# Performance work log

Measured on AMD Instinct MI355X. Metric: run time of the kernel, lower is better.

## Reference

```python
import jax, jax.numpy as jnp
import numpy as np

EMBED_DIM = 128
B, N = 8, 2048


def entmax15(z):
    """Exact 1.5-entmax along the last axis (Peters & Martins 2019, sort-based)."""
    z = z / 2.0
    z = z - jnp.max(z, axis=-1, keepdims=True)  # shift-invariance -> numerical stability
    zs = -jnp.sort(-z, axis=-1)                 # descending sort
    n = z.shape[-1]
    k = jnp.arange(1, n + 1, dtype=z.dtype)
    mean = jnp.cumsum(zs, axis=-1) / k
    meansq = jnp.cumsum(zs * zs, axis=-1) / k
    ss = k * (meansq - mean * mean)
    delta = (1.0 - ss) / k
    delta_safe = jnp.where(delta > 0, delta, 1.0)
    tau = mean - jnp.where(delta > 0, jnp.sqrt(delta_safe), 0.0)
    support = jnp.sum((tau <= zs).astype(jnp.int32), axis=-1, keepdims=True)
    tau_star = jnp.take_along_axis(tau, support - 1, axis=-1)
    return jnp.square(jnp.maximum(z - tau_star, 0.0))


def setup_inputs() -> dict:
    key = jax.random.key(0)
    ks = jax.random.split(key, 6)
    s = 1.0 / np.sqrt(EMBED_DIM)  # torch nn.Linear default init range
    return {
        "x_c": jax.random.normal(ks[0], (B, N, EMBED_DIM), jnp.float32),
        "x_n": jax.random.normal(ks[1], (B, N, EMBED_DIM), jnp.float32),
        "Wq": jax.random.uniform(ks[2], (EMBED_DIM, EMBED_DIM), jnp.float32, -s, s),
        "bq": jax.random.uniform(ks[3], (EMBED_DIM,), jnp.float32, -s, s),
        "Wk": jax.random.uniform(ks[4], (EMBED_DIM, EMBED_DIM), jnp.float32, -s, s),
        "bk": jax.random.uniform(ks[5], (EMBED_DIM,), jnp.float32, -s, s),
    }


def reference(x_c, x_n, Wq, bq, Wk, bk):
    Q = x_c @ Wq.T + bq                      # [B,N,D]
    K = x_n @ Wk.T + bk                      # [B,N,D]
    A = jnp.einsum("bnd,bmd->bnm", Q, K) / jnp.sqrt(jnp.float32(EMBED_DIM))
    # entmax15 sparse normalization over keys; dropout is identity in eval mode
    return entmax15(A)
```

## Files before the change

kernel.cpp:

```cpp
#include <hip/hip_runtime.h>
#include <hip/hip_bf16.h>

#define BATCH 8
#define SEQ   2048
#define DIM   128
#define NROWS 16384
#define THETA_SPAN 22.62741699796952f

typedef __bf16    bf16x8   __attribute__((ext_vector_type(8)));
typedef float     floatx16 __attribute__((ext_vector_type(16)));
typedef _Float16  half2v   __attribute__((ext_vector_type(2)));

static __device__ __forceinline__ unsigned short f2bf(float v) {
    union { __hip_bfloat16 h; unsigned short u; } c;
    c.h = __float2bfloat16(v);
    return c.u;
}
static __device__ __forceinline__ float bf2f(unsigned short u) {
    union { unsigned int i; float f; } c;
    c.i = (unsigned int)u << 16;
    return c.f;
}
static __device__ __forceinline__ unsigned short f2h(float v) {
    union { _Float16 h; unsigned short u; } c;
    c.h = (_Float16)v;
    return c.u;
}

#if __has_builtin(__builtin_amdgcn_fdot2)
static __device__ __forceinline__ float fdot2acc(half2v a, half2v b, float c) {
    return __builtin_amdgcn_fdot2(a, b, c, false);
}
#else
static __device__ __forceinline__ float fdot2acc(half2v a, half2v b, float c) {
    return fmaf((float)a.y, (float)b.y, fmaf((float)a.x, (float)b.x, c));
}
#endif

__global__ void __launch_bounds__(256)
proj_qk(const float* __restrict__ xq, const float* __restrict__ xn,
        const float* __restrict__ Wq, const float* __restrict__ bq,
        const float* __restrict__ Wk, const float* __restrict__ bk,
        unsigned short* __restrict__ Qhi, unsigned short* __restrict__ Qlo,
        unsigned short* __restrict__ Kb) {
    const int isK = blockIdx.y;
    const float* __restrict__ X    = isK ? xn : xq;
    const float* __restrict__ W    = isK ? Wk : Wq;
    const float* __restrict__ bias = isK ? bk : bq;

    __shared__ float wt[64][133];
    __shared__ float xs[64][68];
    const int tid  = threadIdx.x;
    const int l    = tid & 15;
    const int kthi = tid >> 4;
    const int row0 = blockIdx.x * 64;

    float s[4][8];
#pragma unroll
    for (int rr = 0; rr < 4; ++rr)
#pragma unroll
        for (int j = 0; j < 8; ++j) s[rr][j] = 0.0f;

    for (int ph = 0; ph < 2; ++ph) {
        const int e0 = ph * 64;
#pragma unroll
        for (int i = 0; i < 8; ++i) {
            const int g  = tid + 256 * i;
            const int d  = g >> 4;
            const int c4 = g & 15;
            float4 wv = *reinterpret_cast<const float4*>(
                W + (size_t)d * DIM + e0 + 4 * c4);
            wt[4*c4+0][d] = wv.x;  wt[4*c4+1][d] = wv.y;
            wt[4*c4+2][d] = wv.z;  wt[4*c4+3][d] = wv.w;
        }
#pragma unroll
        for (int i = 0; i < 4; ++i) {
            const int g  = tid + 256 * i;
            const int r  = g >> 4;
            const int c4 = g & 15;
            float4 xv = *reinterpret_cast<const float4*>(
                X + (size_t)(row0 + r) * DIM + e0 + 4 * c4);
            *reinterpret_cast<float4*>(&xs[r][4 * c4]) = xv;
        }
        __syncthreads();
#pragma unroll 8
        for (int e = 0; e < 64; ++e) {
            float w8[8];
            *reinterpret_cast<float4*>(w8)     =
                *reinterpret_cast<const float4*>(&wt[e][kthi * 8]);
            *reinterpret_cast<float4*>(w8 + 4) =
                *reinterpret_cast<const float4*>(&wt[e][kthi * 8 + 4]);
#pragma unroll
            for (int rr = 0; rr < 4; ++rr) {
                const float xv = xs[l + 16 * rr][e];
#pragma unroll
                for (int j = 0; j < 8; ++j) s[rr][j] = fmaf(xv, w8[j], s[rr][j]);
            }
        }
        __syncthreads();
    }

    float b8[8];
    *reinterpret_cast<float4*>(b8)     = *reinterpret_cast<const float4*>(bias + kthi * 8);
    *reinterpret_cast<float4*>(b8 + 4) = *reinterpret_cast<const float4*>(bias + kthi * 8 + 4);

    if (!isK) {
#pragma unroll
        for (int rr = 0; rr < 4; ++rr) {
            const int row = row0 + l + 16 * rr;
            union { uint4 v; unsigned short u[8]; } ph_, pl_;
#pragma unroll
            for (int j = 0; j < 8; ++j) {
                const float v = s[rr][j] + b8[j];
                const unsigned short h = f2bf(v);
                ph_.u[j] = h;
                pl_.u[j] = f2bf(v - bf2f(h));
            }
            const size_t base = ((size_t)kthi * NROWS + row) * 8;
            *reinterpret_cast<uint4*>(Qhi + base) = ph_.v;
            *reinterpret_cast<uint4*>(Qlo + base) = pl_.v;
        }
    } else {
#pragma unroll
        for (int rr = 0; rr < 4; ++rr) {
            const int row = row0 + l + 16 * rr;
            const int b   = row >> 11;
            const int key = row & (SEQ - 1);
            union { uint4 v; unsigned short u[8]; } pk;
#pragma unroll
            for (int j = 0; j < 8; ++j) pk.u[j] = f2bf(s[rr][j] + b8[j]);
            const size_t base = (((size_t)(b * 16) + kthi) * SEQ + key) * 8;
            *reinterpret_cast<uint4*>(Kb + base) = pk.v;
        }
    }
}

__global__ void __launch_bounds__(1024, 4)
attn_fused(const __bf16* __restrict__ Qhi, const __bf16* __restrict__ Qlo,
           const __bf16* __restrict__ Kb, float* __restrict__ out) {
    __shared__ uint2 S4[8][SEQ];
    const int tid  = threadIdx.x;
    const int wv   = tid >> 6;
    const int lane = tid & 63;
    const int l5   = lane & 31;
    const int hi5  = lane >> 5;
    const int row0 = blockIdx.x * 32;
    const int b    = row0 >> 11;
    const int key0 = wv * 128;

    {
        floatx16 acc[4];
        const floatx16 zerov = {};
#pragma unroll
        for (int t = 0; t < 4; ++t) acc[t] = zerov;

        const __bf16* qh = Qhi + ((size_t)hi5 * NROWS + row0 + l5) * 8;
        const __bf16* ql = Qlo + ((size_t)hi5 * NROWS + row0 + l5) * 8;
        const __bf16* kp = Kb + (((size_t)(b * 16) + hi5) * SEQ + key0 + l5) * 8;
        const size_t qstep = (size_t)2 * NROWS * 8;
        const size_t kstep = (size_t)2 * SEQ * 8;

#pragma unroll
        for (int kt = 0; kt < 8; ++kt) {
            const bf16x8 ah = *reinterpret_cast<const bf16x8*>(qh + kt * qstep);
            const bf16x8 al = *reinterpret_cast<const bf16x8*>(ql + kt * qstep);
            const __bf16* kc = kp + kt * kstep;
#pragma unroll
            for (int t = 0; t < 4; ++t) {
                const bf16x8 bkv = *reinterpret_cast<const bf16x8*>(kc + (size_t)t * 256);
                acc[t] = __builtin_amdgcn_mfma_f32_32x32x16_bf16(ah, bkv, acc[t], 0, 0, 0);
                acc[t] = __builtin_amdgcn_mfma_f32_32x32x16_bf16(al, bkv, acc[t], 0, 0, 0);
            }
        }
#pragma unroll
        for (int t = 0; t < 4; ++t) {
#pragma unroll
            for (int a = 0; a < 4; ++a) {
                union { uint2 v; unsigned short u[4]; } pk;
#pragma unroll
                for (int bb = 0; bb < 4; ++bb) pk.u[bb] = f2h(acc[t][4 * a + bb]);
                S4[2 * a + hi5][key0 + t * 32 + l5] = pk.v;
            }
        }
    }
    __syncthreads();

    const int g  = wv >> 1;
    const int sp = wv & 1;

    const unsigned int* Sw = reinterpret_cast<const unsigned int*>(&S4[g][0]);
    unsigned int raw[32];
#pragma unroll
    for (int c = 0; c < 32; ++c) raw[c] = Sw[2 * (c * 64 + lane) + sp];

    const half2v hzero = {(_Float16)0.0f, (_Float16)0.0f};

#pragma unroll
    for (int s = 0; s < 2; ++s) {
        half2v z[16];
#pragma unroll
        for (int i = 0; i < 16; ++i) {
            const unsigned int merged = __builtin_amdgcn_perm(
                raw[2 * i + 1], raw[2 * i],
                s ? 0x07060302u : 0x05040100u);
            union { unsigned int u; half2v h; } cv;
            cv.u = merged;
            z[i] = cv.h;
        }

        float m = -1e30f;
#pragma unroll
        for (int i = 0; i < 16; ++i)
            m = fmaxf(m, fmaxf((float)z[i].x, (float)z[i].y));
#pragma unroll
        for (int off = 32; off >= 1; off >>= 1)
            m = fmaxf(m, __shfl_xor(m, off, 64));

        float lo = m - THETA_SPAN, hi = m;
        float th = 0.0f;
        for (int it = 0; it < 11; ++it) {
            th = 0.5f * (lo + hi);
            const _Float16 thh = (_Float16)th;
            const half2v nth2 = {(_Float16)-thh, (_Float16)-thh};
            float f = 0.0f;
#pragma unroll
            for (int i = 0; i < 16; ++i) {
                half2v d = z[i] + nth2;
                d = __builtin_elementwise_max(d, hzero);
                f = fdot2acc(d, d, f);
            }
#pragma unroll
            for (int off = 32; off >= 1; off >>= 1)
                f += __shfl_xor(f, off, 64);
            if (f >= 512.0f) lo = th; else hi = th;
        }
        th = 0.5f * (lo + hi);
        th = (float)((_Float16)th);

        float* orow = out + (size_t)(row0 + 4 * g + 2 * sp + s) * SEQ + lane;
#pragma unroll
        for (int i = 0; i < 16; ++i) {
            const float d0 = fmaxf((float)z[i].x - th, 0.0f);
            const float d1 = fmaxf((float)z[i].y - th, 0.0f);
            orow[(size_t)(2 * i) * 64]     = d0 * d0 * (1.0f / 512.0f);
            orow[(size_t)(2 * i + 1) * 64] = d1 * d1 * (1.0f / 512.0f);
        }
    }
}

extern "C" void kernel_launch(void* const* d_in, const int* in_sizes, int n_in,
                              void* d_out, int out_size, void* d_ws, size_t ws_size,
                              hipStream_t stream) {
    const float* x_c = (const float*)d_in[0];
    const float* x_n = (const float*)d_in[1];
    const float* Wq  = (const float*)d_in[2];
    const float* bq  = (const float*)d_in[3];
    const float* Wk  = (const float*)d_in[4];
    const float* bk  = (const float*)d_in[5];
    float* out = (float*)d_out;

    char* ws = (char*)d_ws;
    unsigned short* Qhi = (unsigned short*)ws;
    unsigned short* Qlo = (unsigned short*)(ws + ((size_t)4 << 20));
    unsigned short* Kbl = (unsigned short*)(ws + ((size_t)8 << 20));

    proj_qk<<<dim3(NROWS / 64, 2), 256, 0, stream>>>(
        x_c, x_n, Wq, bq, Wk, bk, Qhi, Qlo, Kbl);
    attn_fused<<<NROWS / 32, 1024, 0, stream>>>(
        (const __bf16*)Qhi, (const __bf16*)Qlo, (const __bf16*)Kbl, out);
}
```

Measured before the change: 200.7 us.

## Switch to 16-row blocks with 16x16x32 MFMA and interleaved bisection of two rows

The attention kernel now processes 16 query rows per block with 512 threads instead of 32 rows with 1024 threads, using 16x16x32 bf16 MFMA tiles over 256 keys per wave. The fp16 score buffer moves to a padded flat LDS layout, which cuts LDS per block and should let more blocks fit per CU. Each wave also runs the bisection for its two rows interleaved, so the cross-lane reductions of the two rows can overlap instead of running back to back. The cost is more K reloads across blocks, since K is reused by fewer query rows per block, and more register pressure from holding both rows at once.

```diff
diff --git a/kernel.cpp b/kernel.cpp
--- a/kernel.cpp
+++ b/kernel.cpp
@@ -8,7 +8,7 @@
 #define THETA_SPAN 22.62741699796952f
 
 typedef __bf16    bf16x8   __attribute__((ext_vector_type(8)));
-typedef float     floatx16 __attribute__((ext_vector_type(16)));
+typedef float     floatx4  __attribute__((ext_vector_type(4)));
 typedef _Float16  half2v   __attribute__((ext_vector_type(2)));
 
 static __device__ __forceinline__ unsigned short f2bf(float v) {
@@ -135,52 +135,49 @@
     }
 }
 
-__global__ void __launch_bounds__(1024, 4)
+__global__ void __launch_bounds__(512, 4)
 attn_fused(const __bf16* __restrict__ Qhi, const __bf16* __restrict__ Qlo,
            const __bf16* __restrict__ Kb, float* __restrict__ out) {
-    __shared__ uint2 S4[8][SEQ];
+    __shared__ unsigned int SW[4 * 4098];
     const int tid  = threadIdx.x;
     const int wv   = tid >> 6;
     const int lane = tid & 63;
-    const int l5   = lane & 31;
-    const int hi5  = lane >> 5;
-    const int row0 = blockIdx.x * 32;
+    const int l4   = lane & 15;
+    const int quad = lane >> 4;
+    const int row0 = blockIdx.x * 16;
     const int b    = row0 >> 11;
-    const int key0 = wv * 128;
+    const int key0 = wv * 256;
 
     {
-        floatx16 acc[4];
-        const floatx16 zerov = {};
-#pragma unroll
-        for (int t = 0; t < 4; ++t) acc[t] = zerov;
-
-        const __bf16* qh = Qhi + ((size_t)hi5 * NROWS + row0 + l5) * 8;
-        const __bf16* ql = Qlo + ((size_t)hi5 * NROWS + row0 + l5) * 8;
-        const __bf16* kp = Kb + (((size_t)(b * 16) + hi5) * SEQ + key0 + l5) * 8;
-        const size_t qstep = (size_t)2 * NROWS * 8;
-        const size_t kstep = (size_t)2 * SEQ * 8;
-
-#pragma unroll
-        for (int kt = 0; kt < 8; ++kt) {
-            const bf16x8 ah = *reinterpret_cast<const bf16x8*>(qh + kt * qstep);
-            const bf16x8 al = *reinterpret_cast<const bf16x8*>(ql + kt * qstep);
-            const __bf16* kc = kp + kt * kstep;
-#pragma unroll
-            for (int t = 0; t < 4; ++t) {
-                const bf16x8 bkv = *reinterpret_cast<const bf16x8*>(kc + (size_t)t * 256);
-                acc[t] = __builtin_amdgcn_mfma_f32_32x32x16_bf16(ah, bkv, acc[t], 0, 0, 0);
-                acc[t] = __builtin_amdgcn_mfma_f32_32x32x16_bf16(al, bkv, acc[t], 0, 0, 0);
+        floatx4 acc[16];
+        const floatx4 zerov = {};
+#pragma unroll
+        for (int t = 0; t < 16; ++t) acc[t] = zerov;
+
+        const size_t qbase = ((size_t)quad * NROWS + row0 + l4) * 8;
+        const size_t kbase = (((size_t)(b * 16) + quad) * SEQ + key0 + l4) * 8;
+        const size_t qstep = (size_t)4 * NROWS * 8;
+        const size_t kstep = (size_t)4 * SEQ * 8;
+
+#pragma unroll
+        for (int kt = 0; kt < 4; ++kt) {
+            const bf16x8 ah = *reinterpret_cast<const bf16x8*>(Qhi + qbase + kt * qstep);
+            const bf16x8 al = *reinterpret_cast<const bf16x8*>(Qlo + qbase + kt * qstep);
+            const __bf16* kc = Kb + kbase + kt * kstep;
+#pragma unroll
+            for (int t = 0; t < 16; ++t) {
+                const bf16x8 bkv = *reinterpret_cast<const bf16x8*>(kc + (size_t)t * 128);
+                acc[t] = __builtin_amdgcn_mfma_f32_16x16x32_bf16(ah, bkv, acc[t], 0, 0, 0);
+                acc[t] = __builtin_amdgcn_mfma_f32_16x16x32_bf16(al, bkv, acc[t], 0, 0, 0);
             }
         }
 #pragma unroll
-        for (int t = 0; t < 4; ++t) {
-#pragma unroll
-            for (int a = 0; a < 4; ++a) {
-                union { uint2 v; unsigned short u[4]; } pk;
-#pragma unroll
-                for (int bb = 0; bb < 4; ++bb) pk.u[bb] = f2h(acc[t][4 * a + bb]);
-                S4[2 * a + hi5][key0 + t * 32 + l5] = pk.v;
-            }
+        for (int t = 0; t < 16; ++t) {
+            union { uint2 v; unsigned short u[4]; } pk;
+#pragma unroll
+            for (int bb = 0; bb < 4; ++bb) pk.u[bb] = f2h(acc[t][bb]);
+            const int key = key0 + t * 16 + l4;
+            *reinterpret_cast<uint2*>(&SW[quad * 4098 + 2 * key]) = pk.v;
         }
     }
     __syncthreads();
@@ -188,63 +185,79 @@
     const int g  = wv >> 1;
     const int sp = wv & 1;
 
-    const unsigned int* Sw = reinterpret_cast<const unsigned int*>(&S4[g][0]);
+    const unsigned int* Sw = &SW[g * 4098];
     unsigned int raw[32];
 #pragma unroll
     for (int c = 0; c < 32; ++c) raw[c] = Sw[2 * (c * 64 + lane) + sp];
 
+    half2v z0[16], z1[16];
+#pragma unroll
+    for (int i = 0; i < 16; ++i) {
+        union { unsigned int u; half2v h; } c0, c1;
+        c0.u = __builtin_amdgcn_perm(raw[2 * i + 1], raw[2 * i], 0x05040100u);
+        c1.u = __builtin_amdgcn_perm(raw[2 * i + 1], raw[2 * i], 0x07060302u);
+        z0[i] = c0.h;
+        z1[i] = c1.h;
+    }
+
     const half2v hzero = {(_Float16)0.0f, (_Float16)0.0f};
 
-#pragma unroll
-    for (int s = 0; s < 2; ++s) {
-        half2v z[16];
+    float m0 = -1e30f, m1 = -1e30f;
+#pragma unroll
+    for (int i = 0; i < 16; ++i) {
+        m0 = fmaxf(m0, fmaxf((float)z0[i].x, (float)z0[i].y));
+        m1 = fmaxf(m1, fmaxf((float)z1[i].x, (float)z1[i].y));
+    }
+#pragma unroll
+    for (int off = 32; off >= 1; off >>= 1) {
+        m0 = fmaxf(m0, __shfl_xor(m0, off, 64));
+        m1 = fmaxf(m1, __shfl_xor(m1, off, 64));
+    }
+
+    float lo0 = m0 - THETA_SPAN, hi0 = m0;
+    float lo1 = m1 - THETA_SPAN, hi1 = m1;
+    for (int it = 0; it < 11; ++it) {
+        const float th0 = 0.5f * (lo0 + hi0);
+        const float th1 = 0.5f * (lo1 + hi1);
+        const _Float16 t0h = (_Float16)th0;
+        const _Float16 t1h = (_Float16)th1;
+        const half2v n0 = {(_Float16)-t0h, (_Float16)-t0h};
+        const half2v n1 = {(_Float16)-t1h, (_Float16)-t1h};
+        float f0 = 0.0f, f1 = 0.0f;
 #pragma unroll
         for (int i = 0; i < 16; ++i) {
-            const unsigned int merged = __builtin_amdgcn_perm(
-                raw[2 * i + 1], raw[2 * i],
-                s ? 0x07060302u : 0x05040100u);
-            union { unsigned int u; half2v h; } cv;
-            cv.u = merged;
-            z[i] = cv.h;
-        }
-
-        float m = -1e30f;
-#pragma unroll
-        for (int i = 0; i < 16; ++i)
-            m = fmaxf(m, fmaxf((float)z[i].x, (float)z[i].y));
-#pragma unroll
-        for (int off = 32; off >= 1; off >>= 1)
-            m = fmaxf(m, __shfl_xor(m, off, 64));
-
-        float lo = m - THETA_SPAN, hi = m;
-        float th = 0.0f;
-        for (int it = 0; it < 11; ++it) {
-            th = 0.5f * (lo + hi);
-            const _Float16 thh = (_Float16)th;
-            const half2v nth2 = {(_Float16)-thh, (_Float16)-thh};
-            float f = 0.0f;
-#pragma unroll
-            for (int i = 0; i < 16; ++i) {
-                half2v d = z[i] + nth2;
-                d = __builtin_elementwise_max(d, hzero);
-                f = fdot2acc(d, d, f);
-            }
-#pragma unroll
-            for (int off = 32; off >= 1; off >>= 1)
-                f += __shfl_xor(f, off, 64);
-            if (f >= 512.0f) lo = th; else hi = th;
-        }
-        th = 0.5f * (lo + hi);
-        th = (float)((_Float16)th);
-
-        float* orow = out + (size_t)(row0 + 4 * g + 2 * sp + s) * SEQ + lane;
-#pragma unroll
-        for (int i = 0; i < 16; ++i) {
-            const float d0 = fmaxf((float)z[i].x - th, 0.0f);
-            const float d1 = fmaxf((float)z[i].y - th, 0.0f);
-            orow[(size_t)(2 * i) * 64]     = d0 * d0 * (1.0f / 512.0f);
-            orow[(size_t)(2 * i + 1) * 64] = d1 * d1 * (1.0f / 512.0f);
-        }
+            half2v d0 = z0[i] + n0;
+            half2v d1 = z1[i] + n1;
+            d0 = __builtin_elementwise_max(d0, hzero);
+            d1 = __builtin_elementwise_max(d1, hzero);
+            f0 = fdot2acc(d0, d0, f0);
+            f1 = fdot2acc(d1, d1, f1);
+        }
+#pragma unroll
+        for (int off = 32; off >= 1; off >>= 1) {
+            f0 += __shfl_xor(f0, off, 64);
+            f1 += __shfl_xor(f1, off, 64);
+        }
+        if (f0 >= 512.0f) lo0 = th0; else hi0 = th0;
+        if (f1 >= 512.0f) lo1 = th1; else hi1 = th1;
+    }
+    float th0 = 0.5f * (lo0 + hi0);
+    float th1 = 0.5f * (lo1 + hi1);
+    th0 = (float)((_Float16)th0);
+    th1 = (float)((_Float16)th1);
+
+    float* o0 = out + (size_t)(row0 + 4 * g + 2 * sp + 0) * SEQ + lane;
+    float* o1 = out + (size_t)(row0 + 4 * g + 2 * sp + 1) * SEQ + lane;
+#pragma unroll
+    for (int i = 0; i < 16; ++i) {
+        const float a0 = fmaxf((float)z0[i].x - th0, 0.0f);
+        const float a1 = fmaxf((float)z0[i].y - th0, 0.0f);
+        const float b0 = fmaxf((float)z1[i].x - th1, 0.0f);
+        const float b1 = fmaxf((float)z1[i].y - th1, 0.0f);
+        o0[(size_t)(2 * i) * 64]     = a0 * a0 * (1.0f / 512.0f);
+        o0[(size_t)(2 * i + 1) * 64] = a1 * a1 * (1.0f / 512.0f);
+        o1[(size_t)(2 * i) * 64]     = b0 * b0 * (1.0f / 512.0f);
+        o1[(size_t)(2 * i + 1) * 64] = b1 * b1 * (1.0f / 512.0f);
     }
 }
 
@@ -266,6 +279,6 @@
 
     proj_qk<<<dim3(NROWS / 64, 2), 256, 0, stream>>>(
         x_c, x_n, Wq, bq, Wk, bk, Qhi, Qlo, Kbl);
-    attn_fused<<<NROWS / 32, 1024, 0, stream>>>(
+    attn_fused<<<NROWS / 16, 512, 0, stream>>>(
         (const __bf16*)Qhi, (const __bf16*)Qlo, (const __bf16*)Kbl, out);
 }
```

Measured after the change: 200.7 us. Within noise of the previous version (+0.0%).
